# Kernel tuning notes

Hardware: AMD Instinct MI355X
Metric: run time of the kernel (lower is better)

## Reference

```python
import jax, jax.numpy as jnp
import numpy as np

H = 16
D_K = 64
HALF_WINDOW = 256  # window_size // 2 = 512 // 2


def setup_inputs() -> dict:
    key = jax.random.key(0)
    ks = jax.random.split(key, 9)
    B, S, D = 2, 2048, 1024
    scale = 0.02
    return {
        "x": jax.random.normal(ks[0], (B, S, D), dtype=jnp.float32),
        "Wq": jax.random.normal(ks[1], (D, D), dtype=jnp.float32) * scale,
        "bq": jax.random.normal(ks[2], (D,), dtype=jnp.float32) * scale,
        "Wk": jax.random.normal(ks[3], (D, D), dtype=jnp.float32) * scale,
        "bk": jax.random.normal(ks[4], (D,), dtype=jnp.float32) * scale,
        "Wv": jax.random.normal(ks[5], (D, D), dtype=jnp.float32) * scale,
        "bv": jax.random.normal(ks[6], (D,), dtype=jnp.float32) * scale,
        "Wo": jax.random.normal(ks[7], (D, D), dtype=jnp.float32) * scale,
        "bo": jax.random.normal(ks[8], (D,), dtype=jnp.float32) * scale,
    }


def reference(x, Wq, bq, Wk, bk, Wv, bv, Wo, bo):
    B, S, D = x.shape
    # projections -> [B, H, S, d_k]
    q = (x @ Wq + bq).reshape(B, S, H, D_K).transpose(0, 2, 1, 3)
    k = (x @ Wk + bk).reshape(B, S, H, D_K).transpose(0, 2, 1, 3)
    v = (x @ Wv + bv).reshape(B, S, H, D_K).transpose(0, 2, 1, 3)
    # dense scores, as in the original module
    scores = jnp.einsum("bhqd,bhkd->bhqk", q, k) / jnp.sqrt(jnp.float32(D_K))
    # sliding window band mask: 0 inside |i-j| <= half_window, -inf outside
    idx = jnp.arange(S)
    band = jnp.abs(idx[:, None] - idx[None, :]) <= HALF_WINDOW  # [S, S]
    window_mask = jnp.where(band, jnp.float32(0.0), -jnp.inf)
    scores = scores + window_mask[None, None, :, :]
    attn = jax.nn.softmax(scores, axis=-1)  # dropout is identity (p=0 / eval)
    out = jnp.einsum("bhqk,bhkd->bhqd", attn, v)  # [B, H, S, d_k]
    out = out.transpose(0, 2, 1, 3).reshape(B, S, D)
    return out @ Wo + bo
```

## Files before the change

### kernel.cpp

```cpp
#include <hip/hip_runtime.h>
#include <hip/hip_bf16.h>
#include <cstdint>
#include <cstddef>

using bf16 = __hip_bfloat16;
typedef __attribute__((ext_vector_type(8))) short bf16x8v;
typedef __attribute__((ext_vector_type(4))) float f32x4v;
typedef __attribute__((ext_vector_type(16))) float f32x16v;
typedef __attribute__((ext_vector_type(4))) int i32x4v;

__device__ __forceinline__ f32x4v mfma16x16x32(bf16x8v a, bf16x8v b, f32x4v c) {
  return __builtin_amdgcn_mfma_f32_16x16x32_bf16(a, b, c, 0, 0, 0);
}
__device__ __forceinline__ f32x16v mfma32x32x16(bf16x8v a, bf16x8v b, f32x16v c) {
  return __builtin_amdgcn_mfma_f32_32x32x16_bf16(a, b, c, 0, 0, 0);
}

__device__ __forceinline__ void lds_async16(const void* g, void* l) {
  __builtin_amdgcn_global_load_lds(
      (__attribute__((address_space(1))) void*)g,
      (__attribute__((address_space(3))) void*)l, 16, 0, 0);
}

__device__ __forceinline__ unsigned short f2bf_bits(float f) {
  union { bf16 h; unsigned short u; } cv;
  cv.h = __float2bfloat16(f);
  return cv.u;
}
__device__ __forceinline__ uint32_t pk_bf2(float a, float b) {
  return (uint32_t)f2bf_bits(a) | ((uint32_t)f2bf_bits(b) << 16);
}

#define QSC 0.18033688011111793f


__global__ void convert_x_k(const float* __restrict__ x, bf16* __restrict__ xb) {
  const int i = blockIdx.x * blockDim.x + threadIdx.x;
  const float4 v = reinterpret_cast<const float4*>(x)[i];
  ushort4 o;
  o.x = f2bf_bits(v.x); o.y = f2bf_bits(v.y);
  o.z = f2bf_bits(v.z); o.w = f2bf_bits(v.w);
  reinterpret_cast<ushort4*>(xb)[i] = o;
}

__global__ void transpose_w_k(const float* __restrict__ Wq, const float* __restrict__ Wk,
                              const float* __restrict__ Wv, const float* __restrict__ Wo,
                              bf16* __restrict__ wcat, bf16* __restrict__ wot) {
  __shared__ float tile[64][65];
  const int mat = blockIdx.z;
  const float* W = (mat == 0) ? Wq : (mat == 1) ? Wk : (mat == 2) ? Wv : Wo;
  bf16* dst = (mat < 3) ? (wcat + (size_t)mat * 1024 * 1024) : wot;
  const int n0 = blockIdx.x * 64, k0 = blockIdx.y * 64;
  const int tr = threadIdx.x >> 6, tc = threadIdx.x & 63;
#pragma unroll
  for (int it = 0; it < 16; ++it)
    tile[it * 4 + tr][tc] = W[(size_t)(k0 + it * 4 + tr) * 1024 + n0 + tc];
  __syncthreads();
#pragma unroll
  for (int it = 0; it < 16; ++it) {
    const int n = n0 + it * 4 + tr;
    dst[(size_t)n * 1024 + k0 + tc] = __float2bfloat16(tile[tc][it * 4 + tr]);
  }
}

__global__ void build_bias_k(const float* __restrict__ bq, const float* __restrict__ bk,
                             const float* __restrict__ bv, float* __restrict__ bcat) {
  const int i = blockIdx.x * 256 + threadIdx.x;
  if (i < 3072)
    bcat[i] = (i < 1024) ? bq[i] : (i < 2048) ? bk[i - 1024] : bv[i - 2048];
}

template <int EPI>
__global__ __launch_bounds__(256, 3) void gemm_k(
    const bf16* __restrict__ A, const bf16* __restrict__ Bt,
    const float* __restrict__ bias,
    bf16* __restrict__ qb, bf16* __restrict__ kb, bf16* __restrict__ vtb,
    float* __restrict__ outf)
{
  constexpr int K = 1024;
  __shared__ bf16 As[128 * 64];
  __shared__ bf16 Bs[128 * 64];
  const int t = threadIdx.x;
  const int lane = t & 63, w = t >> 6;
  const int g = lane >> 4, r = lane & 15;
  const int wr = w >> 1, wc = w & 1;
  const int m0 = blockIdx.x * 128, n0 = blockIdx.y * 128;

  const bf16* aS[4];
  const bf16* bS[4];
  bf16* aD[4];
  bf16* bD[4];
#pragma unroll
  for (int i = 0; i < 4; ++i) {
    const int G = t + 256 * i;
    const int row = G >> 3, gd = G & 7;
    const int col = ((gd ^ (row & 7)) << 3);
    aS[i] = A + (size_t)(m0 + row) * K + col;
    bS[i] = Bt + (size_t)(n0 + row) * K + col;
    aD[i] = As + w * 512 + i * 2048;
    bD[i] = Bs + w * 512 + i * 2048;
  }

  f32x4v acc[4][4] = {};

  for (int kt = 0; kt < 16; ++kt) {
    const int ko = kt * 64;
#pragma unroll
    for (int i = 0; i < 4; ++i) {
      lds_async16(aS[i] + ko, aD[i]);
      lds_async16(bS[i] + ko, bD[i]);
    }
    __syncthreads();

#pragma unroll
    for (int ks = 0; ks < 2; ++ks) {
      const int csw = ((ks * 4 + g) ^ (r & 7)) << 4;
      bf16x8v af[4];
#pragma unroll
      for (int m = 0; m < 4; ++m)
        af[m] = *reinterpret_cast<const bf16x8v*>(
            (const char*)As + (wr * 64 + m * 16 + r) * 128 + csw);
#pragma unroll
      for (int n = 0; n < 4; ++n) {
        const bf16x8v bf_ = *reinterpret_cast<const bf16x8v*>(
            (const char*)Bs + (wc * 64 + n * 16 + r) * 128 + csw);
#pragma unroll
        for (int m = 0; m < 4; ++m)
          acc[m][n] = mfma16x16x32(af[m], bf_, acc[m][n]);
      }
    }
    __syncthreads();
  }

#pragma unroll
  for (int n = 0; n < 4; ++n) {
    const int gcol = n0 + wc * 64 + n * 16 + r;
    const float bv_ = bias[gcol];
    if (EPI == 0) {
      const int mat = gcol >> 10;
      const int d = gcol & 1023;
      const int hh = d >> 6, dk = d & 63;
#pragma unroll
      for (int m = 0; m < 4; ++m) {
#pragma unroll
        for (int v = 0; v < 4; ++v) {
          const int grow = m0 + wr * 64 + m * 16 + g * 4 + v;
          const int b = grow >> 11, s = grow & 2047;
          const float val = acc[m][n][v] + bv_;
          const size_t bh = (size_t)(b * 16 + hh);
          if (mat == 0)      qb[(bh * 2048 + s) * 64 + dk] = __float2bfloat16(val * QSC);
          else if (mat == 1) kb[(bh * 2048 + s) * 64 + dk] = __float2bfloat16(val);
          else               vtb[(bh * 64 + dk) * 2048 + s] = __float2bfloat16(val);
        }
      }
    } else {
#pragma unroll
      for (int m = 0; m < 4; ++m) {
#pragma unroll
        for (int v = 0; v < 4; ++v) {
          const int grow = m0 + wr * 64 + m * 16 + g * 4 + v;
          outf[(size_t)grow * 1024 + gcol] = acc[m][n][v] + bv_;
        }
      }
    }
  }
}

__global__ __launch_bounds__(64) void attn_k(
    const bf16* __restrict__ qb, const bf16* __restrict__ kb_,
    const bf16* __restrict__ vtb, bf16* __restrict__ aout)
{
  constexpr int S = 2048;
  const int lane = threadIdx.x & 63;
  const int hi = lane >> 5, l31 = lane & 31;
  const int d_ = blockIdx.x;
  const int xcd = d_ & 7, slot = d_ >> 3;
  const int bh_i = xcd * 4 + (slot >> 6);
  const int q0 = (slot & 63) * 32;
  const int b = bh_i >> 4, h = bh_i & 15;
  const size_t bh = (size_t)b * 16 + h;
  const bf16* qp = qb + bh * (size_t)(S * 64);
  const bf16* kp = kb_ + bh * (size_t)(S * 64);
  const bf16* vp = vtb + bh * (size_t)(64 * S);

  bf16x8v qf[4];
#pragma unroll
  for (int i = 0; i < 4; ++i)
    qf[i] = *reinterpret_cast<const bf16x8v*>(&qp[(size_t)(q0 + l31) * 64 + i * 16 + hi * 8]);

  f32x16v o0 = {}, o1 = {};
  float lrun = 0.f;

  const int jlo = (q0 >= 256) ? (q0 - 256) : 0;
  const int jend = (q0 + 256 <= S - 32) ? (q0 + 256) : (S - 32);
  const int nIter = ((jend - jlo) >> 5) + 1;

  auto LDK = [&](int j, bf16x8v* kf) {
    const bf16* p0 = kp + (size_t)(j + l31) * 64 + hi * 8;
#pragma unroll
    for (int i = 0; i < 4; ++i)
      kf[i] = *reinterpret_cast<const bf16x8v*>(p0 + i * 16);
  };
  auto LDV = [&](int j, bf16x8v* vf) {
#pragma unroll
    for (int db = 0; db < 2; ++db)
#pragma unroll
      for (int kk = 0; kk < 2; ++kk)
        vf[db * 2 + kk] = *reinterpret_cast<const bf16x8v*>(
            &vp[(size_t)(db * 32 + l31) * S + j + kk * 16 + hi * 8]);
  };

  auto STEP = [&](int idx, bf16x8v* kc, bf16x8v* vc, bf16x8v* kn, bf16x8v* vn) {
    const int j = jlo + idx * 32;
    if (idx + 1 < nIter) { LDK(j + 32, kn); LDV(j + 32, vn); }

    f32x16v s = {};
#pragma unroll
    for (int i = 0; i < 4; ++i) s = mfma32x32x16(kc[i], qf[i], s);

    float p[16];
    const bool needMask = ((q0 + 31 - j) > 256) || ((j + 31 - q0) > 256);
    if (needMask) {
      const int base = l31 - 4 * hi + (q0 - j) + 256;
#pragma unroll
      for (int tt = 0; tt < 4; ++tt)
#pragma unroll
        for (int e = 0; e < 4; ++e) {
          const int kk_ = 8 * tt + e;
          const float ev = __builtin_amdgcn_exp2f(s[4 * tt + e]);
          p[4 * tt + e] = ((unsigned)(base - kk_) <= 512u) ? ev : 0.f;
        }
    } else {
#pragma unroll
      for (int i = 0; i < 16; ++i) p[i] = __builtin_amdgcn_exp2f(s[i]);
    }
    lrun += (((p[0] + p[1]) + (p[2] + p[3])) + ((p[4] + p[5]) + (p[6] + p[7]))) +
            (((p[8] + p[9]) + (p[10] + p[11])) + ((p[12] + p[13]) + (p[14] + p[15])));

    uint32_t W00 = pk_bf2(p[0],  p[1]),  W01 = pk_bf2(p[2],  p[3]);
    uint32_t W10 = pk_bf2(p[4],  p[5]),  W11 = pk_bf2(p[6],  p[7]);
    uint32_t W20 = pk_bf2(p[8],  p[9]),  W21 = pk_bf2(p[10], p[11]);
    uint32_t W30 = pk_bf2(p[12], p[13]), W31 = pk_bf2(p[14], p[15]);
    asm volatile("v_permlane32_swap_b32 %0, %1" : "+v"(W00), "+v"(W10));
    asm volatile("v_permlane32_swap_b32 %0, %1" : "+v"(W01), "+v"(W11));
    asm volatile("v_permlane32_swap_b32 %0, %1" : "+v"(W20), "+v"(W30));
    asm volatile("v_permlane32_swap_b32 %0, %1" : "+v"(W21), "+v"(W31));
    union { i32x4v i; bf16x8v hv; } c0, c1;
    c0.i = (i32x4v){(int)W00, (int)W01, (int)W10, (int)W11};
    c1.i = (i32x4v){(int)W20, (int)W21, (int)W30, (int)W31};
    o0 = mfma32x32x16(vc[0], c0.hv, o0);
    o0 = mfma32x32x16(vc[1], c1.hv, o0);
    o1 = mfma32x32x16(vc[2], c0.hv, o1);
    o1 = mfma32x32x16(vc[3], c1.hv, o1);
  };

  bf16x8v ka[4], va[4], kn2[4], vn2[4];
  LDK(jlo, ka); LDV(jlo, va);
  int it = 0;
  while (it + 2 <= nIter) {
    STEP(it, ka, va, kn2, vn2);
    STEP(it + 1, kn2, vn2, ka, va);
    it += 2;
  }
  if (it < nIter) STEP(it, ka, va, kn2, vn2);

  lrun += __shfl_xor(lrun, 32);
  const float inv = 1.0f / lrun;

  const size_t ob = ((size_t)b * S + q0 + l31) * 1024 + h * 64 + hi * 4;
#pragma unroll
  for (int tt = 0; tt < 4; ++tt) {
    uint2 u;
    u.x = pk_bf2(o0[4 * tt] * inv, o0[4 * tt + 1] * inv);
    u.y = pk_bf2(o0[4 * tt + 2] * inv, o0[4 * tt + 3] * inv);
    *reinterpret_cast<uint2*>(&aout[ob + 8 * tt]) = u;
    uint2 v2;
    v2.x = pk_bf2(o1[4 * tt] * inv, o1[4 * tt + 1] * inv);
    v2.y = pk_bf2(o1[4 * tt + 2] * inv, o1[4 * tt + 3] * inv);
    *reinterpret_cast<uint2*>(&aout[ob + 32 + 8 * tt]) = v2;
  }
}

extern "C" void kernel_launch(void* const* d_in, const int* in_sizes, int n_in,
                              void* d_out, int out_size, void* d_ws, size_t ws_size,
                              hipStream_t stream) {
  (void)in_sizes; (void)n_in; (void)out_size; (void)ws_size;
  const float* x  = (const float*)d_in[0];
  const float* Wq = (const float*)d_in[1];
  const float* bq = (const float*)d_in[2];
  const float* Wk = (const float*)d_in[3];
  const float* bk = (const float*)d_in[4];
  const float* Wv = (const float*)d_in[5];
  const float* bv = (const float*)d_in[6];
  const float* Wo = (const float*)d_in[7];
  const float* bo = (const float*)d_in[8];
  float* out = (float*)d_out;

  char* ws = (char*)d_ws;
  bf16*  xb    = (bf16*)(ws);
  bf16*  wcat  = (bf16*)(ws + 8388608);
  bf16*  wot   = (bf16*)(ws + 14680064);
  bf16*  qbuf  = (bf16*)(ws + 16777216);
  bf16*  kbuf  = (bf16*)(ws + 25165824);
  bf16*  vtbuf = (bf16*)(ws + 33554432);
  bf16*  aoutb = (bf16*)(ws + 41943040);
  float* bcat  = (float*)(ws + 50331648);

  convert_x_k<<<4096, 256, 0, stream>>>(x, xb);
  transpose_w_k<<<dim3(16, 16, 4), 256, 0, stream>>>(Wq, Wk, Wv, Wo, wcat, wot);
  build_bias_k<<<12, 256, 0, stream>>>(bq, bk, bv, bcat);

  gemm_k<0><<<dim3(32, 24), 256, 0, stream>>>(xb, wcat, bcat, qbuf, kbuf, vtbuf, nullptr);
  attn_k<<<2048, 64, 0, stream>>>(qbuf, kbuf, vtbuf, aoutb);
  gemm_k<1><<<dim3(32, 8), 256, 0, stream>>>(aoutb, wot, bo, nullptr, nullptr, nullptr, out);
}
```

Measured before the change: 106.1 us.

## Replace LDS-tiled GEMM with single-wave direct-from-global register double-buffered GEMM

The projection GEMMs change from 256-thread blocks with 128x128 tiles staged through LDS via async global-to-LDS loads to one-wave blocks computing 64x64 tiles that load MFMA operands straight from global memory into registers. Register double-buffering overlaps the next k-step's loads with current MFMAs and removes all barriers. Block indices are remapped across XCDs for locality. The trade-off is no LDS sharing of operands between waves, so global/L2 traffic per FLOP rises and per-lane 16-byte loads are strided across rows.

```diff
diff --git a/kernel.cpp b/kernel.cpp
--- a/kernel.cpp
+++ b/kernel.cpp
@@ -14,12 +14,6 @@
 }
 __device__ __forceinline__ f32x16v mfma32x32x16(bf16x8v a, bf16x8v b, f32x16v c) {
   return __builtin_amdgcn_mfma_f32_32x32x16_bf16(a, b, c, 0, 0, 0);
-}
-
-__device__ __forceinline__ void lds_async16(const void* g, void* l) {
-  __builtin_amdgcn_global_load_lds(
-      (__attribute__((address_space(1))) void*)g,
-      (__attribute__((address_space(3))) void*)l, 16, 0, 0);
 }
 
 __device__ __forceinline__ unsigned short f2bf_bits(float f) {
@@ -71,80 +65,70 @@
 }
 
 template <int EPI>
-__global__ __launch_bounds__(256, 3) void gemm_k(
+__global__ __launch_bounds__(64, 3) void gemmw_k(
     const bf16* __restrict__ A, const bf16* __restrict__ Bt,
     const float* __restrict__ bias,
     bf16* __restrict__ qb, bf16* __restrict__ kb, bf16* __restrict__ vtb,
     float* __restrict__ outf)
 {
   constexpr int K = 1024;
-  __shared__ bf16 As[128 * 64];
-  __shared__ bf16 Bs[128 * 64];
-  const int t = threadIdx.x;
-  const int lane = t & 63, w = t >> 6;
+  constexpr int NT = (EPI == 0) ? 48 : 16;
+  constexpr int NWG = (EPI == 0) ? 3072 : 1024;
+  const int lane = threadIdx.x & 63;
   const int g = lane >> 4, r = lane & 15;
-  const int wr = w >> 1, wc = w & 1;
-  const int m0 = blockIdx.x * 128, n0 = blockIdx.y * 128;
-
-  const bf16* aS[4];
-  const bf16* bS[4];
-  bf16* aD[4];
-  bf16* bD[4];
+
+  const int d = blockIdx.x;
+  const int wg = (d & 7) * (NWG >> 3) + (d >> 3);
+  const int m0 = (wg / NT) * 64, n0 = (wg % NT) * 64;
+
+  const bf16* aB[4];
+  const bf16* bB[4];
 #pragma unroll
   for (int i = 0; i < 4; ++i) {
-    const int G = t + 256 * i;
-    const int row = G >> 3, gd = G & 7;
-    const int col = ((gd ^ (row & 7)) << 3);
-    aS[i] = A + (size_t)(m0 + row) * K + col;
-    bS[i] = Bt + (size_t)(n0 + row) * K + col;
-    aD[i] = As + w * 512 + i * 2048;
-    bD[i] = Bs + w * 512 + i * 2048;
+    aB[i] = A + (size_t)(m0 + i * 16 + r) * K + g * 8;
+    bB[i] = Bt + (size_t)(n0 + i * 16 + r) * K + g * 8;
   }
 
   f32x4v acc[4][4] = {};
-
-  for (int kt = 0; kt < 16; ++kt) {
-    const int ko = kt * 64;
-#pragma unroll
-    for (int i = 0; i < 4; ++i) {
-      lds_async16(aS[i] + ko, aD[i]);
-      lds_async16(bS[i] + ko, bD[i]);
-    }
-    __syncthreads();
-
-#pragma unroll
-    for (int ks = 0; ks < 2; ++ks) {
-      const int csw = ((ks * 4 + g) ^ (r & 7)) << 4;
-      bf16x8v af[4];
-#pragma unroll
-      for (int m = 0; m < 4; ++m)
-        af[m] = *reinterpret_cast<const bf16x8v*>(
-            (const char*)As + (wr * 64 + m * 16 + r) * 128 + csw);
-#pragma unroll
-      for (int n = 0; n < 4; ++n) {
-        const bf16x8v bf_ = *reinterpret_cast<const bf16x8v*>(
-            (const char*)Bs + (wc * 64 + n * 16 + r) * 128 + csw);
-#pragma unroll
-        for (int m = 0; m < 4; ++m)
-          acc[m][n] = mfma16x16x32(af[m], bf_, acc[m][n]);
-      }
-    }
-    __syncthreads();
+  bf16x8v a0[4], b0[4], a1[4], b1[4];
+
+  auto LD = [&](int kt, bf16x8v* af, bf16x8v* bf) {
+#pragma unroll
+    for (int m = 0; m < 4; ++m)
+      af[m] = *reinterpret_cast<const bf16x8v*>(aB[m] + kt * 32);
+#pragma unroll
+    for (int n = 0; n < 4; ++n)
+      bf[n] = *reinterpret_cast<const bf16x8v*>(bB[n] + kt * 32);
+  };
+  auto FM = [&](bf16x8v* af, bf16x8v* bf) {
+#pragma unroll
+    for (int m = 0; m < 4; ++m)
+#pragma unroll
+      for (int n = 0; n < 4; ++n)
+        acc[m][n] = mfma16x16x32(af[m], bf[n], acc[m][n]);
+  };
+
+  LD(0, a0, b0);
+  for (int kt = 0; kt < 32; kt += 2) {
+    LD(kt + 1, a1, b1);
+    FM(a0, b0);
+    if (kt + 2 < 32) LD(kt + 2, a0, b0);
+    FM(a1, b1);
   }
 
 #pragma unroll
   for (int n = 0; n < 4; ++n) {
-    const int gcol = n0 + wc * 64 + n * 16 + r;
+    const int gcol = n0 + n * 16 + r;
     const float bv_ = bias[gcol];
     if (EPI == 0) {
       const int mat = gcol >> 10;
-      const int d = gcol & 1023;
-      const int hh = d >> 6, dk = d & 63;
+      const int dc = gcol & 1023;
+      const int hh = dc >> 6, dk = dc & 63;
 #pragma unroll
       for (int m = 0; m < 4; ++m) {
 #pragma unroll
         for (int v = 0; v < 4; ++v) {
-          const int grow = m0 + wr * 64 + m * 16 + g * 4 + v;
+          const int grow = m0 + m * 16 + g * 4 + v;
           const int b = grow >> 11, s = grow & 2047;
           const float val = acc[m][n][v] + bv_;
           const size_t bh = (size_t)(b * 16 + hh);
@@ -158,7 +142,7 @@
       for (int m = 0; m < 4; ++m) {
 #pragma unroll
         for (int v = 0; v < 4; ++v) {
-          const int grow = m0 + wr * 64 + m * 16 + g * 4 + v;
+          const int grow = m0 + m * 16 + g * 4 + v;
           outf[(size_t)grow * 1024 + gcol] = acc[m][n][v] + bv_;
         }
       }
@@ -310,7 +294,7 @@
   transpose_w_k<<<dim3(16, 16, 4), 256, 0, stream>>>(Wq, Wk, Wv, Wo, wcat, wot);
   build_bias_k<<<12, 256, 0, stream>>>(bq, bk, bv, bcat);
 
-  gemm_k<0><<<dim3(32, 24), 256, 0, stream>>>(xb, wcat, bcat, qbuf, kbuf, vtbuf, nullptr);
+  gemmw_k<0><<<3072, 64, 0, stream>>>(xb, wcat, bcat, qbuf, kbuf, vtbuf, nullptr);
   attn_k<<<2048, 64, 0, stream>>>(qbuf, kbuf, vtbuf, aoutb);
-  gemm_k<1><<<dim3(32, 8), 256, 0, stream>>>(aoutb, wot, bo, nullptr, nullptr, nullptr, out);
-}
+  gemmw_k<1><<<1024, 64, 0, stream>>>(aoutb, wot, bo, nullptr, nullptr, nullptr, out);
+}
```

New measurement: 184.0 us. +73.5%, slower.

## Double-buffer GEMM LDS tiles and stage QKV epilogue through LDS

Applied to the files above, without the earlier changes.

The GEMM main loop now uses two 128x32 LDS buffers. The async global-to-LDS load of the next k-tile is issued before the MFMAs on the current tile, which replaces the two barriers per 64-wide step with one wait and one barrier per 32-wide step. The QKV epilogue writes each wave's 64x64 bf16 tile into LDS, transposed for V, then stores it to global memory with 16-byte vector writes instead of scattered 2-byte writes. The risks are more barriers in total from the halved k-step, and possible LDS bank conflicts in the epilogue's transposed writes.

```diff
diff --git a/kernel.cpp b/kernel.cpp
--- a/kernel.cpp
+++ b/kernel.cpp
@@ -78,82 +78,101 @@
     float* __restrict__ outf)
 {
   constexpr int K = 1024;
-  __shared__ bf16 As[128 * 64];
-  __shared__ bf16 Bs[128 * 64];
+  __shared__ bf16 smem[16384];
   const int t = threadIdx.x;
   const int lane = t & 63, w = t >> 6;
   const int g = lane >> 4, r = lane & 15;
   const int wr = w >> 1, wc = w & 1;
   const int m0 = blockIdx.x * 128, n0 = blockIdx.y * 128;
 
-  const bf16* aS[4];
-  const bf16* bS[4];
-  bf16* aD[4];
-  bf16* bD[4];
-#pragma unroll
-  for (int i = 0; i < 4; ++i) {
-    const int G = t + 256 * i;
-    const int row = G >> 3, gd = G & 7;
-    const int col = ((gd ^ (row & 7)) << 3);
-    aS[i] = A + (size_t)(m0 + row) * K + col;
-    bS[i] = Bt + (size_t)(n0 + row) * K + col;
-    aD[i] = As + w * 512 + i * 2048;
-    bD[i] = Bs + w * 512 + i * 2048;
-  }
+  const int srow = t >> 2;
+  const int scol = ((lane & 3) ^ g) << 3;
+  const bf16* aS0 = A + (size_t)(m0 + srow) * K + scol;
+  const bf16* aS1 = A + (size_t)(m0 + 64 + srow) * K + scol;
+  const bf16* bS0 = Bt + (size_t)(n0 + srow) * K + scol;
+  const bf16* bS1 = Bt + (size_t)(n0 + 64 + srow) * K + scol;
 
   f32x4v acc[4][4] = {};
 
-  for (int kt = 0; kt < 16; ++kt) {
-    const int ko = kt * 64;
-#pragma unroll
-    for (int i = 0; i < 4; ++i) {
-      lds_async16(aS[i] + ko, aD[i]);
-      lds_async16(bS[i] + ko, bD[i]);
-    }
-    __syncthreads();
-
-#pragma unroll
-    for (int ks = 0; ks < 2; ++ks) {
-      const int csw = ((ks * 4 + g) ^ (r & 7)) << 4;
-      bf16x8v af[4];
-#pragma unroll
-      for (int m = 0; m < 4; ++m)
-        af[m] = *reinterpret_cast<const bf16x8v*>(
-            (const char*)As + (wr * 64 + m * 16 + r) * 128 + csw);
-#pragma unroll
-      for (int n = 0; n < 4; ++n) {
-        const bf16x8v bf_ = *reinterpret_cast<const bf16x8v*>(
-            (const char*)Bs + (wc * 64 + n * 16 + r) * 128 + csw);
-#pragma unroll
-        for (int m = 0; m < 4; ++m)
-          acc[m][n] = mfma16x16x32(af[m], bf_, acc[m][n]);
+  auto STAGE = [&](int kt, int buf) {
+    const int ko = kt * 32;
+    char* d0 = (char*)smem + buf * 16384 + w * 1024;
+    lds_async16(aS0 + ko, d0);
+    lds_async16(aS1 + ko, d0 + 4096);
+    lds_async16(bS0 + ko, d0 + 8192);
+    lds_async16(bS1 + ko, d0 + 12288);
+  };
+
+  const int csw = (g ^ ((r >> 2) & 3)) << 4;
+
+  STAGE(0, 0);
+  asm volatile("s_waitcnt vmcnt(0)" ::: "memory");
+  __builtin_amdgcn_s_barrier();
+
+  for (int kt = 0; kt < 32; ++kt) {
+    if (kt < 31) STAGE(kt + 1, (kt + 1) & 1);
+
+    const char* buf = (const char*)smem + (kt & 1) * 16384;
+    bf16x8v af[4], bfr[4];
+#pragma unroll
+    for (int m = 0; m < 4; ++m)
+      af[m] = *reinterpret_cast<const bf16x8v*>(buf + (wr * 64 + m * 16 + r) * 64 + csw);
+#pragma unroll
+    for (int n = 0; n < 4; ++n)
+      bfr[n] = *reinterpret_cast<const bf16x8v*>(buf + 8192 + (wc * 64 + n * 16 + r) * 64 + csw);
+#pragma unroll
+    for (int m = 0; m < 4; ++m)
+#pragma unroll
+      for (int n = 0; n < 4; ++n)
+        acc[m][n] = mfma16x16x32(af[m], bfr[n], acc[m][n]);
+
+    if (kt < 31) asm volatile("s_waitcnt vmcnt(0)" ::: "memory");
+    __builtin_amdgcn_s_barrier();
+  }
+
+  if (EPI == 0) {
+    const int gcol0 = n0 + wc * 64;
+    const int mat = gcol0 >> 10;
+    const int hh = (gcol0 & 1023) >> 6;
+    const int s0 = m0 + wr * 64;
+    const int b_ = s0 >> 11, sb = s0 & 2047;
+    const size_t bh = (size_t)(b_ * 16 + hh);
+    unsigned short* ep = (unsigned short*)smem + w * 4096;
+
+#pragma unroll
+    for (int n = 0; n < 4; ++n) {
+      const int dkl = n * 16 + r;
+      const float bv_ = bias[gcol0 + dkl];
+#pragma unroll
+      for (int m = 0; m < 4; ++m) {
+#pragma unroll
+        for (int v = 0; v < 4; ++v) {
+          const int sl = m * 16 + g * 4 + v;
+          const float val = acc[m][n][v] + bv_;
+          if (mat == 0)      ep[sl * 64 + dkl] = f2bf_bits(val * QSC);
+          else if (mat == 1) ep[sl * 64 + dkl] = f2bf_bits(val);
+          else               ep[dkl * 64 + sl] = f2bf_bits(val);
+        }
       }
     }
-    __syncthreads();
-  }
-
-#pragma unroll
-  for (int n = 0; n < 4; ++n) {
-    const int gcol = n0 + wc * 64 + n * 16 + r;
-    const float bv_ = bias[gcol];
-    if (EPI == 0) {
-      const int mat = gcol >> 10;
-      const int d = gcol & 1023;
-      const int hh = d >> 6, dk = d & 63;
-#pragma unroll
-      for (int m = 0; m < 4; ++m) {
-#pragma unroll
-        for (int v = 0; v < 4; ++v) {
-          const int grow = m0 + wr * 64 + m * 16 + g * 4 + v;
-          const int b = grow >> 11, s = grow & 2047;
-          const float val = acc[m][n][v] + bv_;
-          const size_t bh = (size_t)(b * 16 + hh);
-          if (mat == 0)      qb[(bh * 2048 + s) * 64 + dk] = __float2bfloat16(val * QSC);
-          else if (mat == 1) kb[(bh * 2048 + s) * 64 + dk] = __float2bfloat16(val);
-          else               vtb[(bh * 64 + dk) * 2048 + s] = __float2bfloat16(val);
-        }
-      }
-    } else {
+#pragma unroll
+    for (int i = 0; i < 8; ++i) {
+      const int chunk = i * 64 + lane;
+      const int rw = chunk >> 3;
+      const int off = (chunk & 7) * 8;
+      const bf16x8v vv = *reinterpret_cast<const bf16x8v*>(ep + rw * 64 + off);
+      if (mat == 0)
+        *reinterpret_cast<bf16x8v*>(qb + (bh * 2048 + sb + rw) * 64 + off) = vv;
+      else if (mat == 1)
+        *reinterpret_cast<bf16x8v*>(kb + (bh * 2048 + sb + rw) * 64 + off) = vv;
+      else
+        *reinterpret_cast<bf16x8v*>(vtb + (bh * 64 + rw) * 2048 + sb + off) = vv;
+    }
+  } else {
+#pragma unroll
+    for (int n = 0; n < 4; ++n) {
+      const int gcol = n0 + wc * 64 + n * 16 + r;
+      const float bv_ = bias[gcol];
 #pragma unroll
       for (int m = 0; m < 4; ++m) {
 #pragma unroll
```

New measurement: 105.4 us. Within noise of the previous version (-0.6%).
